# Optimization experiments

Measured on AMD Instinct MI355X. Metric: run time of the kernel, lower is better.

## Reference

```python
import jax, jax.numpy as jnp
import numpy as np

B, S, D, H, M = 4, 2048, 1024, 16, 128
DH = D // H
SCALE = jnp.float32(np.sqrt(D / H))


def setup_inputs() -> dict:
    key = jax.random.key(0)
    ks = jax.random.split(key, 4)
    x = jax.random.normal(ks[0], (B, S, D), dtype=jnp.float32)
    mask = jnp.zeros((B, 1, 1, S), dtype=bool)
    W_in = jax.random.normal(ks[1], (3 * D, D), dtype=jnp.float32) * 0.02
    b_in = jnp.zeros((3 * D,), dtype=jnp.float32)
    pos_emb = jax.random.normal(ks[2], (2 * M + 1, DH), dtype=jnp.float32)
    W_out = jax.random.normal(ks[3], (D, D), dtype=jnp.float32) * 0.02
    b_out = jnp.zeros((D,), dtype=jnp.float32)
    return {"x": x, "mask": mask, "W_in": W_in, "b_in": b_in,
            "pos_emb": pos_emb, "W_out": W_out, "b_out": b_out}


def _arrange_pos(pos_emb, seq_len, max_len):
    k = jnp.arange(seq_len)
    q = jnp.arange(seq_len)
    idx = jnp.clip(k[None, :] - q[:, None], -max_len, max_len) + max_len  # [S,S]
    return pos_emb[idx]  # [S,S,DH]


def reference(x, mask, W_in, b_in, pos_emb, W_out, b_out):
    b, s, d = x.shape
    qkv = x @ W_in.T + b_in                      # [B,S,3D]
    qkv = qkv.reshape(b, s, H, 3 * DH).transpose(0, 2, 1, 3)  # [B,H,S,3DH]
    Q, K, V = jnp.split(qkv, 3, axis=3)          # each [B,H,S,DH]
    logits = jnp.einsum('bhqd,bhkd->bhqk', Q, K)
    rel = _arrange_pos(pos_emb, s, M)            # [S,S,DH] (q,k,dh)
    pos_logits = jnp.einsum('bhqd,qkd->bhqk', Q, rel)
    logits = (logits + pos_logits) / SCALE
    logits = jnp.where(mask, -jnp.inf, logits)
    attn = jax.nn.softmax(logits, axis=3)
    combined = jnp.einsum('bhqk,bhkd->bhqd', attn, V)
    out = combined.transpose(0, 2, 1, 3).reshape(b, s, d)  # concat heads
    return out @ W_out.T + b_out
```

## Files before the change

kernel.cpp:

```cpp
#include <hip/hip_runtime.h>
#include <hip/hip_bf16.h>
#include <math.h>

#define SS 2048
#define HH 16
#define NPOS 257
#define C_SCALE 0.18033688f
#define P_THR 256.0f

typedef short  s16x8 __attribute__((ext_vector_type(8)));
typedef float  f32x4 __attribute__((ext_vector_type(4)));
typedef unsigned u32x4 __attribute__((ext_vector_type(4)));

__device__ __forceinline__ unsigned short f2bf(float f) {
    unsigned u = __builtin_bit_cast(unsigned, f);
    u += 0x7fff + ((u >> 16) & 1);
    return (unsigned short)(u >> 16);
}
__device__ __forceinline__ float bf2f(unsigned short b) {
    return __builtin_bit_cast(float, (unsigned)b << 16);
}
__device__ __forceinline__ s16x8 pack8(float4 a, float4 b) {
    s16x8 v;
    v[0]=(short)f2bf(a.x); v[1]=(short)f2bf(a.y); v[2]=(short)f2bf(a.z); v[3]=(short)f2bf(a.w);
    v[4]=(short)f2bf(b.x); v[5]=(short)f2bf(b.y); v[6]=(short)f2bf(b.z); v[7]=(short)f2bf(b.w);
    return v;
}
__device__ __forceinline__ unsigned cvtpk(float lo, float hi) {
    unsigned r;
    asm("v_cvt_pk_bf16_f32 %0, %1, %2" : "=v"(r) : "v"(lo), "v"(hi));
    return r;
}
__device__ __forceinline__ float exp2_fast(float x) {
    float r;
    asm("v_exp_f32 %0, %1" : "=v"(r) : "v"(x));
    return r;
}
__device__ __forceinline__ f32x4 mfma16(s16x8 a, s16x8 b, f32x4 c) {
    return __builtin_amdgcn_mfma_f32_16x16x32_bf16(a, b, c, 0, 0, 0);
}
__device__ __forceinline__ void gload_lds16(const void* gsrc, void* ldst) {
    __builtin_amdgcn_global_load_lds(
        (const __attribute__((address_space(1))) unsigned int*)gsrc,
        (__attribute__((address_space(3))) unsigned int*)ldst,
        16, 0, 0);
}
__device__ __forceinline__ int colp(int k) {
    return ((k >> 5) << 6) | (((k >> 2) & 3) << 4) | (((k >> 4) & 1) << 3) | ((k & 3) << 1);
}

__global__ __launch_bounds__(256)
void cvt_bf16(const float* __restrict__ in, unsigned short* __restrict__ out, int n8)
{
    for (int i = blockIdx.x * blockDim.x + threadIdx.x; i < n8; i += gridDim.x * blockDim.x) {
        const float4* p = (const float4*)(in + (size_t)i * 8);
        *(s16x8*)(out + (size_t)i * 8) = pack8(p[0], p[1]);
    }
}

__global__ __launch_bounds__(256)
void gemm_bf16_nt(const unsigned short* __restrict__ A,
                  const unsigned short* __restrict__ Bm,
                  const float* __restrict__ bias, float* __restrict__ Cout,
                  int Ndim, int Kdim)
{
    __shared__ short As[128 * 32];
    __shared__ short Bs[128 * 32];
    const int tid  = threadIdx.x;
    const int lane = tid & 63;
    const int wv   = tid >> 6;
    const int g    = lane >> 4;
    const int ln   = lane & 15;
    const int wm   = wv >> 1, wn = wv & 1;
    const int tm   = blockIdx.y << 7, tn = blockIdx.x << 7;
    const int srow  = lane >> 2;
    const int sslot = lane & 3;

    f32x4 acc[4][4];
#pragma unroll
    for (int mi = 0; mi < 4; ++mi)
#pragma unroll
        for (int ni = 0; ni < 4; ++ni) acc[mi][ni] = f32x4{0.f, 0.f, 0.f, 0.f};

    const unsigned short* Ab = A  + (size_t)(tm + wv*32 + srow) * Kdim + sslot*8;
    const unsigned short* Bb = Bm + (size_t)(tn + wv*32 + srow) * Kdim + sslot*8;
    const size_t rstep16 = (size_t)16 * Kdim;
    char* lA = (char*)As + (wv*32) * 64;
    char* lB = (char*)Bs + (wv*32) * 64;

    for (int k0 = 0; k0 < Kdim; k0 += 32) {
        __syncthreads();
        gload_lds16(Ab + k0,           lA);
        gload_lds16(Ab + k0 + rstep16, lA + 1024);
        gload_lds16(Bb + k0,           lB);
        gload_lds16(Bb + k0 + rstep16, lB + 1024);
        __syncthreads();

        s16x8 af[4], bf_[4];
#pragma unroll
        for (int mi = 0; mi < 4; ++mi)
            af[mi] = *(const s16x8*)((char*)As + (wm*64 + mi*16 + ln)*64 + g*16);
#pragma unroll
        for (int ni = 0; ni < 4; ++ni)
            bf_[ni] = *(const s16x8*)((char*)Bs + (wn*64 + ni*16 + ln)*64 + g*16);
#pragma unroll
        for (int mi = 0; mi < 4; ++mi)
#pragma unroll
            for (int ni = 0; ni < 4; ++ni)
                acc[mi][ni] = mfma16(af[mi], bf_[ni], acc[mi][ni]);
    }

#pragma unroll
    for (int ni = 0; ni < 4; ++ni) {
        const int col = tn + wn*64 + ni*16 + ln;
        const float bcol = bias[col];
#pragma unroll
        for (int mi = 0; mi < 4; ++mi)
#pragma unroll
            for (int j = 0; j < 4; ++j) {
                const int row = tm + wm*64 + mi*16 + 4*g + j;
                Cout[(size_t)row * Ndim + col] = acc[mi][ni][j] + bcol;
            }
    }
}

__global__ __launch_bounds__(256)
void gemm_qkv(const unsigned short* __restrict__ A,
              const unsigned short* __restrict__ Bm,
              const float* __restrict__ bias,
              unsigned short* __restrict__ qb,
              char* __restrict__ kbuf, char* __restrict__ vbuf)
{
    __shared__ short As[128 * 32];
    __shared__ short Bs[128 * 32];
    const int tid  = threadIdx.x;
    const int lane = tid & 63;
    const int wv   = tid >> 6;
    const int g    = lane >> 4;
    const int ln   = lane & 15;
    const int wm   = wv >> 1, wn = wv & 1;
    const int tm   = blockIdx.y << 7, tn = blockIdx.x << 7;
    const int srow  = lane >> 2;
    const int sslot = lane & 3;
    const int Kdim = 1024;

    f32x4 acc[4][4];
#pragma unroll
    for (int mi = 0; mi < 4; ++mi)
#pragma unroll
        for (int ni = 0; ni < 4; ++ni) acc[mi][ni] = f32x4{0.f, 0.f, 0.f, 0.f};

    const unsigned short* Ab = A  + (size_t)(tm + wv*32 + srow) * Kdim + sslot*8;
    const unsigned short* Bb = Bm + (size_t)(tn + wv*32 + srow) * Kdim + sslot*8;
    const size_t rstep16 = (size_t)16 * Kdim;
    char* lA = (char*)As + (wv*32) * 64;
    char* lB = (char*)Bs + (wv*32) * 64;

    for (int k0 = 0; k0 < Kdim; k0 += 32) {
        __syncthreads();
        gload_lds16(Ab + k0,           lA);
        gload_lds16(Ab + k0 + rstep16, lA + 1024);
        gload_lds16(Bb + k0,           lB);
        gload_lds16(Bb + k0 + rstep16, lB + 1024);
        __syncthreads();

        s16x8 af[4], bf_[4];
#pragma unroll
        for (int mi = 0; mi < 4; ++mi)
            af[mi] = *(const s16x8*)((char*)As + (wm*64 + mi*16 + ln)*64 + g*16);
#pragma unroll
        for (int ni = 0; ni < 4; ++ni)
            bf_[ni] = *(const s16x8*)((char*)Bs + (wn*64 + ni*16 + ln)*64 + g*16);
#pragma unroll
        for (int mi = 0; mi < 4; ++mi)
#pragma unroll
            for (int ni = 0; ni < 4; ++ni)
                acc[mi][ni] = mfma16(af[mi], bf_[ni], acc[mi][ni]);
    }

#pragma unroll
    for (int ni = 0; ni < 4; ++ni) {
        const int col  = tn + wn*64 + ni*16 + ln;
        const int col0 = tn + wn*64 + ni*16;
        const int h    = col0 / 192;
        const int r0   = col0 - h*192;
        const int r    = r0 + ln;
        const float bcol = bias[col];
#pragma unroll
        for (int mi = 0; mi < 4; ++mi) {
            const int rowb = tm + wm*64 + mi*16 + 4*g;
            const int bb = rowb >> 11, sl = rowb & 2047;
            const int kt = sl >> 6, kr = sl & 63;
            const size_t tile = ((size_t)(bb*HH + h)*32 + kt) * 8192;
            if (r0 < 64) {
                unsigned short* qp = qb + (((size_t)(bb*HH + h))*SS + sl)*64 + r;
#pragma unroll
                for (int j = 0; j < 4; ++j)
                    qp[(size_t)j*64] = f2bf((acc[mi][ni][j] + bcol) * C_SCALE);
            } else if (r0 < 128) {
                const int d = r - 64;
#pragma unroll
                for (int j = 0; j < 4; ++j) {
                    const int krj = kr + j;
                    *(unsigned short*)(kbuf + tile + krj*128 + ((2*d) ^ ((krj&7)<<4))) =
                        f2bf(acc[mi][ni][j] + bcol);
                }
            } else {
                const int d = r - 128;
                uint2 w;
                w.x = cvtpk(acc[mi][ni][0] + bcol, acc[mi][ni][1] + bcol);
                w.y = cvtpk(acc[mi][ni][2] + bcol, acc[mi][ni][3] + bcol);
                *(uint2*)(vbuf + tile + d*128 + (colp(kr) ^ ((d&7)<<4))) = w;
            }
        }
    }
}

#define FAR_LDS  32768
#define NEAR_LDS (16384 + 64*260*2)

__global__ __launch_bounds__(256, 4)
void attn_far(const unsigned short* __restrict__ qb,
              const char* __restrict__ kbuf, const char* __restrict__ vbuf,
              const unsigned short* __restrict__ pos_bf,
              float* __restrict__ o_state,
              float* __restrict__ m_state,
              float* __restrict__ l_state)
{
    extern __shared__ char smem[];
    char* ksb = smem;
    char* vtb = smem + 16384;

    const int tid = threadIdx.x, lane = tid & 63, wv = tid >> 6;
    const int g = lane >> 4, ln = lane & 15;
    const int fid = ((blockIdx.x & 7) << 7) | (blockIdx.x >> 3);
    const int q0 = (fid & 15) << 7, h = (fid >> 4) & 15, b = fid >> 8;
    const int q0w = q0 + wv*32;
    const int swz = (ln & 7) << 4;

    const unsigned short* qhb = qb + ((size_t)(b*HH + h))*SS*64;
    const char* ktile = kbuf + (size_t)(b*HH + h)*32*8192;
    const char* vtile = vbuf + (size_t)(b*HH + h)*32*8192;

    s16x8 qf[2][2];
#pragma unroll
    for (int gg = 0; gg < 2; ++gg) {
        const unsigned short* qp = qhb + (size_t)(q0w + 16*gg + ln) * 64;
        qf[gg][0] = *(const s16x8*)(qp + 8*g);
        qf[gg][1] = *(const s16x8*)(qp + 32 + 8*g);
    }

    const int ktA = max(0, (q0 - 128) >> 6);
    const int ktB = min(32, (q0 + 256) >> 6);
    const int gap = ktB - ktA, nfar = 32 - gap;

    const int kt0 = (ktA > 0) ? 0 : ktB;
    const char* ksrc = ktile + (size_t)(kt0 + 1 == ktA ? ktB : kt0 + 1)*8192 + wv*2048 + lane*16;
    const char* vsrc = vtile + (size_t)(kt0 + 1 == ktA ? ktB : kt0 + 1)*8192 + wv*2048 + lane*16;
    char* kd0 = ksb + wv*2048;         char* kd1 = kd0 + 8192;
    char* vd0 = vtb + wv*2048;         char* vd1 = vd0 + 8192;
    const char* kb0 = ksb + ln*128 + ((g*16) ^ swz);
    const char* kb1 = ksb + ln*128 + ((64 + g*16) ^ swz);
    const char* vb0 = vtb + ln*128 + ((g*16) ^ swz);
    const char* vb1 = vtb + ln*128 + ((64 + g*16) ^ swz);

    {
        const char* s0k = ktile + (size_t)kt0*8192 + wv*2048 + lane*16;
        const char* s0v = vtile + (size_t)kt0*8192 + wv*2048 + lane*16;
        gload_lds16(s0k, kd0); gload_lds16(s0k + 1024, kd0 + 1024);
        gload_lds16(s0v, vd0); gload_lds16(s0v + 1024, vd0 + 1024);
    }

    float blo[2], bhi[2];
    {
        const int bsrc = (ln >> 2) << 4;
        const int s3 = ln & 3;
#pragma unroll
        for (int pass = 0; pass < 2; ++pass) {
            const int c  = pass*256 + ln;
            const int cc = c > 256 ? 256 : c;
            const unsigned short* pp = pos_bf + (size_t)cc * 64;
            s16x8 b0 = *(const s16x8*)(pp + 8*g);
            s16x8 b1 = *(const s16x8*)(pp + 32 + 8*g);
#pragma unroll
            for (int gg = 0; gg < 2; ++gg) {
                f32x4 d = {0,0,0,0};
                d = mfma16(qf[gg][0], b0, d);
                d = mfma16(qf[gg][1], b1, d);
                const float r0 = __shfl(d[0], bsrc, 64);
                const float r1 = __shfl(d[1], bsrc, 64);
                const float r2 = __shfl(d[2], bsrc, 64);
                const float r3 = __shfl(d[3], bsrc, 64);
                const float r = s3 == 0 ? r0 : s3 == 1 ? r1 : s3 == 2 ? r2 : r3;
                if (pass == 0) blo[gg] = r; else bhi[gg] = r;
            }
        }
    }
    __syncthreads();

    f32x4 o[2][4], l[2];
    float m[2];
#pragma unroll
    for (int gg = 0; gg < 2; ++gg) {
        m[gg] = -INFINITY; l[gg] = f32x4{0,0,0,0};
#pragma unroll
        for (int dt = 0; dt < 4; ++dt) o[gg][dt] = f32x4{0,0,0,0};
    }
    s16x8 ONES;
#pragma unroll
    for (int i = 0; i < 8; ++i) ONES[i] = (short)0x3F80;

#define F_TILE(CUR, vv) do {                                                  \
    if ((vv) + 1 < nfar) {                                                    \
        char* dk_ = (CUR) ? kd0 : kd1;                                        \
        char* dv_ = (CUR) ? vd0 : vd1;                                        \
        gload_lds16(ksrc, dk_); gload_lds16(ksrc + 1024, dk_ + 1024);         \
        gload_lds16(vsrc, dv_); gload_lds16(vsrc + 1024, dv_ + 1024);         \
        const int stp_ = (((vv) + 2) == ktA) ? (gap + 1) * 8192 : 8192;       \
        ksrc += stp_; vsrc += stp_;                                           \
    }                                                                         \
    f32x4 s[2][4];                                                            \
    _Pragma("unroll")                                                         \
    for (int gi = 0; gi < 2; ++gi)                                            \
        _Pragma("unroll")                                                     \
        for (int t = 0; t < 4; ++t) s[gi][t] = f32x4{0,0,0,0};                \
    __builtin_amdgcn_s_setprio(1);                                            \
    _Pragma("unroll")                                                         \
    for (int kc = 0; kc < 2; ++kc) {                                          \
        const char* kbx_ = kc ? kb1 : kb0;                                    \
        s16x8 kf[4];                                                          \
        _Pragma("unroll")                                                     \
        for (int t = 0; t < 4; ++t)                                           \
            kf[t] = *(const s16x8*)(kbx_ + (CUR)*8192 + t*2048);              \
        _Pragma("unroll")                                                     \
        for (int t = 0; t < 4; ++t)                                           \
            _Pragma("unroll")                                                 \
            for (int gi = 0; gi < 2; ++gi)                                    \
                s[gi][t] = mfma16(kf[t], qf[gi][kc], s[gi][t]);               \
    }                                                                         \
    __builtin_amdgcn_s_setprio(0);                                            \
    const bool left_ = (vv) < ktA;                                            \
    u32x4 pa[2][2];                                                           \
    float pmax[2];                                                            \
    _Pragma("unroll")                                                         \
    for (int gi = 0; gi < 2; ++gi) {                                          \
        const float bmv = (left_ ? blo[gi] : bhi[gi]) - m[gi];                \
        float pm = 0.f;                                                       \
        _Pragma("unroll")                                                     \
        for (int t = 0; t < 4; ++t) {                                         \
            const float p0 = exp2_fast(s[gi][t][0] + bmv);                    \
            const float p1 = exp2_fast(s[gi][t][1] + bmv);                    \
            const float p2 = exp2_fast(s[gi][t][2] + bmv);                    \
            const float p3 = exp2_fast(s[gi][t][3] + bmv);                    \
            pm = fmaxf(pm, fmaxf(fmaxf(p0, p1), fmaxf(p2, p3)));              \
            pa[gi][t>>1][2*(t&1)]   = cvtpk(p0, p1);                          \
            pa[gi][t>>1][2*(t&1)+1] = cvtpk(p2, p3);                          \
        }                                                                     \
        pmax[gi] = pm;                                                        \
    }                                                                         \
    if (__any(fmaxf(pmax[0], pmax[1]) > P_THR)) {                             \
        _Pragma("unroll")                                                     \
        for (int gi = 0; gi < 2; ++gi) {                                      \
            const float bc = left_ ? blo[gi] : bhi[gi];                       \
            float mr = s[gi][0][0];                                           \
            _Pragma("unroll")                                                 \
            for (int t = 0; t < 4; ++t)                                       \
                _Pragma("unroll")                                             \
                for (int j = 0; j < 4; ++j) mr = fmaxf(mr, s[gi][t][j]);      \
            mr = fmaxf(mr, __shfl_xor(mr, 16, 64));                           \
            mr = fmaxf(mr, __shfl_xor(mr, 32, 64));                           \
            const float nm = fmaxf(m[gi], mr + bc);                           \
            const float corr = exp2_fast(m[gi] - nm);                         \
            m[gi] = nm;                                                       \
            _Pragma("unroll")                                                 \
            for (int j = 0; j < 4; ++j) {                                     \
                const float cj = __shfl(corr, (lane & 48) + 4*g + j, 64);     \
                _Pragma("unroll")                                             \
                for (int dt = 0; dt < 4; ++dt) o[gi][dt][j] *= cj;            \
                l[gi][j] *= cj;                                               \
            }                                                                 \
            const float nb = bc - nm;                                         \
            _Pragma("unroll")                                                 \
            for (int t = 0; t < 4; ++t) {                                     \
                const float p0 = exp2_fast(s[gi][t][0] + nb);                 \
                const float p1 = exp2_fast(s[gi][t][1] + nb);                 \
                const float p2 = exp2_fast(s[gi][t][2] + nb);                 \
                const float p3 = exp2_fast(s[gi][t][3] + nb);                 \
                pa[gi][t>>1][2*(t&1)]   = cvtpk(p0, p1);                      \
                pa[gi][t>>1][2*(t&1)+1] = cvtpk(p2, p3);                      \
            }                                                                 \
        }                                                                     \
    }                                                                         \
    __builtin_amdgcn_s_setprio(1);                                            \
    _Pragma("unroll")                                                         \
    for (int kc = 0; kc < 2; ++kc) {                                          \
        const char* vbx_ = kc ? vb1 : vb0;                                    \
        _Pragma("unroll")                                                     \
        for (int dt = 0; dt < 4; ++dt) {                                      \
            const s16x8 bv = *(const s16x8*)(vbx_ + (CUR)*8192 + dt*2048);    \
            _Pragma("unroll")                                                 \
            for (int gi = 0; gi < 2; ++gi)                                    \
                o[gi][dt] = mfma16(__builtin_bit_cast(s16x8, pa[gi][kc]), bv, o[gi][dt]); \
        }                                                                     \
        _Pragma("unroll")                                                     \
        for (int gi = 0; gi < 2; ++gi)                                        \
            l[gi] = mfma16(__builtin_bit_cast(s16x8, pa[gi][kc]), ONES, l[gi]); \
    }                                                                         \
    __builtin_amdgcn_s_setprio(0);                                            \
    __syncthreads();                                                          \
} while (0)

    for (int v = 0; v < nfar; v += 2) {
        F_TILE(0, v);
        F_TILE(1, v + 1);
    }

    const size_t rbase = (((size_t)(b*HH + h)) << 11) + q0w;
#pragma unroll
    for (int gg = 0; gg < 2; ++gg) {
        if (lane < 16) m_state[rbase + 16*gg + ln] = m[gg];
        if (ln == 0) {
#pragma unroll
            for (int j = 0; j < 4; ++j) l_state[rbase + 16*gg + 4*g + j] = l[gg][j];
        }
#pragma unroll
        for (int dt = 0; dt < 4; ++dt)
#pragma unroll
            for (int j = 0; j < 4; ++j)
                o_state[(rbase + 16*gg + 4*g + j)*64 + dt*16 + ln] = o[gg][dt][j];
    }
}

__global__ __launch_bounds__(256, 3)
void attn_near(const unsigned short* __restrict__ qb,
               const char* __restrict__ kbuf, const char* __restrict__ vbuf,
               const unsigned short* __restrict__ pos_bf,
               const float* __restrict__ o_state,
               const float* __restrict__ m_state,
               const float* __restrict__ l_state,
               unsigned short* __restrict__ comb)
{
    extern __shared__ char smem[];
    char* ksb = smem;
    unsigned short* tab = (unsigned short*)(smem + 16384);

    const int tid = threadIdx.x, lane = tid & 63, wv = tid >> 6;
    const int g = lane >> 4, ln = lane & 15;
    const int fid = ((blockIdx.x & 7) << 8) | (blockIdx.x >> 3);
    const int q0 = (fid & 31) << 6, h = (fid >> 5) & 15, b = fid >> 9;
    const int q0w = q0 + wv*16;
    const int swz = (ln & 7) << 4;

    const unsigned short* qhb = qb + ((size_t)(b*HH + h))*SS*64;
    const char* ktile = kbuf + (size_t)(b*HH + h)*32*8192;
    const char* vtile = vbuf + (size_t)(b*HH + h)*32*8192;

    s16x8 qf[2];
    {
        const unsigned short* qp = qhb + (size_t)(q0w + ln) * 64;
        qf[0] = *(const s16x8*)(qp + 8*g);
        qf[1] = *(const s16x8*)(qp + 32 + 8*g);
    }

    const int q0p = q0 & ~127;
    const int ktA = max(0, (q0p - 128) >> 6);
    const int ktB = min(32, (q0p + 256) >> 6);
    const int ntile = ktB - ktA;

    const char* ksrcN = ktile + (size_t)(ktA + 1)*8192 + wv*2048 + lane*16;
    char* nkd0 = ksb + wv*2048;        char* nkd1 = nkd0 + 8192;
    const char* kb0 = ksb + ln*128 + ((g*16) ^ swz);
    const char* kb1 = ksb + ln*128 + ((64 + g*16) ^ swz);
    const char* vsr0 = vtile + (size_t)ktA*8192 + ln*128 + ((g*16) ^ swz) + 4096;
    const char* vsr1 = vtile + (size_t)ktA*8192 + ln*128 + ((64 + g*16) ^ swz) + 4096;

    s16x8 vf[8];

    {
        const char* s0 = ktile + (size_t)ktA*8192 + wv*2048 + lane*16;
        gload_lds16(s0, nkd0); gload_lds16(s0 + 1024, nkd0 + 1024);
#pragma unroll
        for (int dt = 0; dt < 4; ++dt) {
            vf[dt]     = *(const s16x8*)(vsr0 + dt*2048 - 4096);
            vf[4 + dt] = *(const s16x8*)(vsr1 + dt*2048 - 4096);
        }
        vsr0 += 8192; vsr1 += 8192;
    }

    for (int ct = 0; ct < 17; ++ct) {
        const int c  = ct*16 + ln;
        const int cc = c > 256 ? 256 : c;
        const unsigned short* pp = pos_bf + (size_t)cc * 64;
        s16x8 b0 = *(const s16x8*)(pp + 8*g);
        s16x8 b1 = *(const s16x8*)(pp + 32 + 8*g);
        f32x4 d = {0,0,0,0};
        d = mfma16(qf[0], b0, d);
        d = mfma16(qf[1], b1, d);
        if (c < NPOS) {
#pragma unroll
            for (int j = 0; j < 4; ++j)
                tab[(16*wv + 4*g + j)*260 + c] = f2bf(d[j]);
        }
    }
    __syncthreads();

    const size_t rbase = (((size_t)(b*HH + h)) << 11) + q0w;
    float m_run = m_state[rbase + ln];
    f32x4 l_acc;
#pragma unroll
    for (int j = 0; j < 4; ++j) l_acc[j] = l_state[rbase + 4*g + j];
    f32x4 o_acc[4];
#pragma unroll
    for (int dt = 0; dt < 4; ++dt)
#pragma unroll
        for (int j = 0; j < 4; ++j)
            o_acc[dt][j] = o_state[(rbase + 4*g + j)*64 + dt*16 + ln];

    const int rowb = (16*wv + ln) * 260;
    const int coff = 4*g - 16*wv - ln + 128 - q0;
    s16x8 ONES;
#pragma unroll
    for (int i = 0; i < 8; ++i) ONES[i] = (short)0x3F80;

#define N_TILE(CUR, vv) do {                                                  \
    if ((vv) + 1 < ntile) {                                                   \
        char* d_ = (CUR) ? nkd0 : nkd1;                                       \
        gload_lds16(ksrcN, d_); gload_lds16(ksrcN + 1024, d_ + 1024);         \
        ksrcN += 8192;                                                        \
    }                                                                         \
    f32x4 s[4];                                                               \
    _Pragma("unroll")                                                         \
    for (int t = 0; t < 4; ++t) s[t] = f32x4{0,0,0,0};                        \
    __builtin_amdgcn_s_setprio(1);                                            \
    _Pragma("unroll")                                                         \
    for (int kc = 0; kc < 2; ++kc) {                                          \
        const char* kbx_ = kc ? kb1 : kb0;                                    \
        s16x8 kf[4];                                                          \
        _Pragma("unroll")                                                     \
        for (int t = 0; t < 4; ++t)                                           \
            kf[t] = *(const s16x8*)(kbx_ + (CUR)*8192 + t*2048);              \
        _Pragma("unroll")                                                     \
        for (int t = 0; t < 4; ++t)                                           \
            s[t] = mfma16(kf[t], qf[kc], s[t]);                               \
    }                                                                         \
    __builtin_amdgcn_s_setprio(0);                                            \
    const int colb = ((ktA + (vv)) << 6) + coff;                              \
    _Pragma("unroll")                                                         \
    for (int t = 0; t < 4; ++t)                                               \
        _Pragma("unroll")                                                     \
        for (int j = 0; j < 4; ++j) {                                         \
            int c = colb + 16*t + j;                                          \
            c = c < 0 ? 0 : (c > 256 ? 256 : c);                              \
            s[t][j] = s[t][j] + bf2f(tab[rowb + c]);                          \
        }                                                                     \
    u32x4 pa[2];                                                              \
    float pm = 0.f;                                                           \
    _Pragma("unroll")                                                         \
    for (int t = 0; t < 4; ++t) {                                             \
        const float p0 = exp2_fast(s[t][0] - m_run);                          \
        const float p1 = exp2_fast(s[t][1] - m_run);                          \
        const float p2 = exp2_fast(s[t][2] - m_run);                          \
        const float p3 = exp2_fast(s[t][3] - m_run);                          \
        pm = fmaxf(pm, fmaxf(fmaxf(p0, p1), fmaxf(p2, p3)));                  \
        pa[t>>1][2*(t&1)]   = cvtpk(p0, p1);                                  \
        pa[t>>1][2*(t&1)+1] = cvtpk(p2, p3);                                  \
    }                                                                         \
    if (__any(pm > P_THR)) {                                                  \
        float mr = s[0][0];                                                   \
        _Pragma("unroll")                                                     \
        for (int t = 0; t < 4; ++t)                                           \
            _Pragma("unroll")                                                 \
            for (int j = 0; j < 4; ++j) mr = fmaxf(mr, s[t][j]);              \
        mr = fmaxf(mr, __shfl_xor(mr, 16, 64));                               \
        mr = fmaxf(mr, __shfl_xor(mr, 32, 64));                               \
        const float nm = fmaxf(m_run, mr);                                    \
        const float corr = exp2_fast(m_run - nm);                             \
        m_run = nm;                                                           \
        _Pragma("unroll")                                                     \
        for (int j = 0; j < 4; ++j) {                                         \
            const float cj = __shfl(corr, (lane & 48) + 4*g + j, 64);         \
            _Pragma("unroll")                                                 \
            for (int dt = 0; dt < 4; ++dt) o_acc[dt][j] *= cj;                \
            l_acc[j] *= cj;                                                   \
        }                                                                     \
        _Pragma("unroll")                                                     \
        for (int t = 0; t < 4; ++t) {                                         \
            const float p0 = exp2_fast(s[t][0] - m_run);                      \
            const float p1 = exp2_fast(s[t][1] - m_run);                      \
            const float p2 = exp2_fast(s[t][2] - m_run);                      \
            const float p3 = exp2_fast(s[t][3] - m_run);                      \
            pa[t>>1][2*(t&1)]   = cvtpk(p0, p1);                              \
            pa[t>>1][2*(t&1)+1] = cvtpk(p2, p3);                              \
        }                                                                     \
    }                                                                         \
    __builtin_amdgcn_s_setprio(1);                                            \
    _Pragma("unroll")                                                         \
    for (int kc = 0; kc < 2; ++kc) {                                          \
        const s16x8 pA_ = __builtin_bit_cast(s16x8, pa[kc]);                  \
        _Pragma("unroll")                                                     \
        for (int dt = 0; dt < 4; ++dt)                                        \
            o_acc[dt] = mfma16(pA_, vf[kc*4 + dt], o_acc[dt]);                \
        l_acc = mfma16(pA_, ONES, l_acc);                                     \
    }                                                                         \
    __builtin_amdgcn_s_setprio(0);                                            \
    if ((vv) + 1 < ntile) {                                                   \
        _Pragma("unroll")                                                     \
        for (int dt = 0; dt < 4; ++dt) {                                      \
            vf[dt]     = *(const s16x8*)(vsr0 + dt*2048 - 4096);              \
            vf[4 + dt] = *(const s16x8*)(vsr1 + dt*2048 - 4096);              \
        }                                                                     \
        vsr0 += 8192; vsr1 += 8192;                                           \
    }                                                                         \
    __syncthreads();                                                          \
} while (0)

    for (int v = 0; v < ntile; v += 2) {
        N_TILE(0, v);
        N_TILE(1, v + 1);
    }

    f32x4 inv;
#pragma unroll
    for (int j = 0; j < 4; ++j) inv[j] = 1.0f / l_acc[j];
#pragma unroll
    for (int dt = 0; dt < 4; ++dt)
#pragma unroll
        for (int j = 0; j < 4; ++j)
            comb[((size_t)b*SS + q0w + 4*g + j)*1024 + h*64 + dt*16 + ln] =
                f2bf(o_acc[dt][j] * inv[j]);
}

extern "C" void kernel_launch(void* const* d_in, const int* in_sizes, int n_in,
                              void* d_out, int out_size, void* d_ws, size_t ws_size,
                              hipStream_t stream)
{
    const float* x     = (const float*)d_in[0];
    const float* W_in  = (const float*)d_in[2];
    const float* b_in  = (const float*)d_in[3];
    const float* pos   = (const float*)d_in[4];
    const float* W_out = (const float*)d_in[5];
    const float* b_out = (const float*)d_in[6];
    float* out = (float*)d_out;

    char* ws = (char*)d_ws;
    unsigned short* q_buf   = (unsigned short*)(ws);
    char*           k_buf   = (char*)          (ws +  16777216);
    char*           v_buf   = (char*)          (ws +  33554432);
    unsigned short* comb_bf = (unsigned short*)(ws +  50331648);
    unsigned short* x_bf    = (unsigned short*)(ws +  67108864);
    unsigned short* wi_bf   = (unsigned short*)(ws +  83886080);
    unsigned short* wo_bf   = (unsigned short*)(ws +  90177536);
    unsigned short* pos_bf  = (unsigned short*)(ws +  92274688);
    float*          o_state = (float*)        (ws +  92340224);
    float*          m_state = (float*)        (ws + 125894656);
    float*          l_state = (float*)        (ws + 126418944);

    cvt_bf16<<<2048, 256, 0, stream>>>(x,     x_bf,  8192*1024/8);
    cvt_bf16<<<1024, 256, 0, stream>>>(W_in,  wi_bf, 3072*1024/8);
    cvt_bf16<<<512,  256, 0, stream>>>(W_out, wo_bf, 1024*1024/8);
    cvt_bf16<<<9,    256, 0, stream>>>(pos,   pos_bf, 2056);

    gemm_qkv<<<dim3(24, 64), 256, 0, stream>>>(x_bf, wi_bf, b_in, q_buf, k_buf, v_buf);

    (void)hipFuncSetAttribute((const void*)attn_far,
                              hipFuncAttributeMaxDynamicSharedMemorySize, FAR_LDS);
    attn_far<<<dim3(1024), 256, FAR_LDS, stream>>>(q_buf, k_buf, v_buf, pos_bf,
                                                   o_state, m_state, l_state);

    (void)hipFuncSetAttribute((const void*)attn_near,
                              hipFuncAttributeMaxDynamicSharedMemorySize, NEAR_LDS);
    attn_near<<<dim3(2048), 256, NEAR_LDS, stream>>>(q_buf, k_buf, v_buf, pos_bf,
                                                     o_state, m_state, l_state, comb_bf);

    gemm_bf16_nt<<<dim3(8, 64), 256, 0, stream>>>(comb_bf, wo_bf, b_out, out, 1024, 1024);
}
```

Baseline: 250.6 us.

## Software-pipeline far attention so PV of previous tile overlaps QK softmax

Restructures the far-range attention loop so the P·V MFMAs for tile v-1 are issued right after the QK^T MFMAs for tile v, before the exp/softmax of tile v. This lets matrix-core work overlap the transcendental and VALU softmax work, which previously ran serially. V now uses a triple-buffered LDS ring, so FAR_LDS grows from 32 KB to 40 KB, and a drain step after the loop finishes the last tile. The probabilities of the previous tile must stay live in registers, which raises register pressure and may affect occupancy at the 4-block launch bound.

```diff
diff --git a/kernel.cpp b/kernel.cpp
--- a/kernel.cpp
+++ b/kernel.cpp
@@ -216,7 +216,7 @@
     }
 }
 
-#define FAR_LDS  32768
+#define FAR_LDS  40960
 #define NEAR_LDS (16384 + 64*260*2)
 
 __global__ __launch_bounds__(256, 4)
@@ -255,20 +255,21 @@
     const int gap = ktB - ktA, nfar = 32 - gap;
 
     const int kt0 = (ktA > 0) ? 0 : ktB;
-    const char* ksrc = ktile + (size_t)(kt0 + 1 == ktA ? ktB : kt0 + 1)*8192 + wv*2048 + lane*16;
-    const char* vsrc = vtile + (size_t)(kt0 + 1 == ktA ? ktB : kt0 + 1)*8192 + wv*2048 + lane*16;
-    char* kd0 = ksb + wv*2048;         char* kd1 = kd0 + 8192;
-    char* vd0 = vtb + wv*2048;         char* vd1 = vd0 + 8192;
-    const char* kb0 = ksb + ln*128 + ((g*16) ^ swz);
-    const char* kb1 = ksb + ln*128 + ((64 + g*16) ^ swz);
-    const char* vb0 = vtb + ln*128 + ((g*16) ^ swz);
-    const char* vb1 = vtb + ln*128 + ((64 + g*16) ^ swz);
+    const int kt1 = (kt0 + 1 == ktA) ? ktB : kt0 + 1;
+    const char* ksrc = ktile + (size_t)kt1*8192 + wv*2048 + lane*16;
+    const char* vsrc = vtile + (size_t)kt1*8192 + wv*2048 + lane*16;
+    const char* kbse0 = ksb + ln*128 + ((g*16) ^ swz);
+    const char* kbse1 = ksb + ln*128 + ((64 + g*16) ^ swz);
+    const char* vbse0 = vtb + ln*128 + ((g*16) ^ swz);
+    const char* vbse1 = vtb + ln*128 + ((64 + g*16) ^ swz);
 
     {
         const char* s0k = ktile + (size_t)kt0*8192 + wv*2048 + lane*16;
         const char* s0v = vtile + (size_t)kt0*8192 + wv*2048 + lane*16;
-        gload_lds16(s0k, kd0); gload_lds16(s0k + 1024, kd0 + 1024);
-        gload_lds16(s0v, vd0); gload_lds16(s0v + 1024, vd0 + 1024);
+        char* dk = ksb + wv*2048;
+        char* dv = vtb + wv*2048;
+        gload_lds16(s0k, dk); gload_lds16(s0k + 1024, dk + 1024);
+        gload_lds16(s0v, dv); gload_lds16(s0v + 1024, dv + 1024);
     }
 
     float blo[2], bhi[2];
@@ -310,110 +311,128 @@
 #pragma unroll
     for (int i = 0; i < 8; ++i) ONES[i] = (short)0x3F80;
 
-#define F_TILE(CUR, vv) do {                                                  \
-    if ((vv) + 1 < nfar) {                                                    \
-        char* dk_ = (CUR) ? kd0 : kd1;                                        \
-        char* dv_ = (CUR) ? vd0 : vd1;                                        \
-        gload_lds16(ksrc, dk_); gload_lds16(ksrc + 1024, dk_ + 1024);         \
-        gload_lds16(vsrc, dv_); gload_lds16(vsrc + 1024, dv_ + 1024);         \
-        const int stp_ = (((vv) + 2) == ktA) ? (gap + 1) * 8192 : 8192;       \
-        ksrc += stp_; vsrc += stp_;                                           \
-    }                                                                         \
-    f32x4 s[2][4];                                                            \
-    _Pragma("unroll")                                                         \
-    for (int gi = 0; gi < 2; ++gi)                                            \
-        _Pragma("unroll")                                                     \
-        for (int t = 0; t < 4; ++t) s[gi][t] = f32x4{0,0,0,0};                \
-    __builtin_amdgcn_s_setprio(1);                                            \
-    _Pragma("unroll")                                                         \
-    for (int kc = 0; kc < 2; ++kc) {                                          \
-        const char* kbx_ = kc ? kb1 : kb0;                                    \
-        s16x8 kf[4];                                                          \
-        _Pragma("unroll")                                                     \
-        for (int t = 0; t < 4; ++t)                                           \
-            kf[t] = *(const s16x8*)(kbx_ + (CUR)*8192 + t*2048);              \
-        _Pragma("unroll")                                                     \
-        for (int t = 0; t < 4; ++t)                                           \
-            _Pragma("unroll")                                                 \
-            for (int gi = 0; gi < 2; ++gi)                                    \
-                s[gi][t] = mfma16(kf[t], qf[gi][kc], s[gi][t]);               \
-    }                                                                         \
-    __builtin_amdgcn_s_setprio(0);                                            \
-    const bool left_ = (vv) < ktA;                                            \
-    u32x4 pa[2][2];                                                           \
-    float pmax[2];                                                            \
-    _Pragma("unroll")                                                         \
-    for (int gi = 0; gi < 2; ++gi) {                                          \
-        const float bmv = (left_ ? blo[gi] : bhi[gi]) - m[gi];                \
-        float pm = 0.f;                                                       \
-        _Pragma("unroll")                                                     \
-        for (int t = 0; t < 4; ++t) {                                         \
-            const float p0 = exp2_fast(s[gi][t][0] + bmv);                    \
-            const float p1 = exp2_fast(s[gi][t][1] + bmv);                    \
-            const float p2 = exp2_fast(s[gi][t][2] + bmv);                    \
-            const float p3 = exp2_fast(s[gi][t][3] + bmv);                    \
-            pm = fmaxf(pm, fmaxf(fmaxf(p0, p1), fmaxf(p2, p3)));              \
-            pa[gi][t>>1][2*(t&1)]   = cvtpk(p0, p1);                          \
-            pa[gi][t>>1][2*(t&1)+1] = cvtpk(p2, p3);                          \
-        }                                                                     \
-        pmax[gi] = pm;                                                        \
-    }                                                                         \
-    if (__any(fmaxf(pmax[0], pmax[1]) > P_THR)) {                             \
-        _Pragma("unroll")                                                     \
-        for (int gi = 0; gi < 2; ++gi) {                                      \
-            const float bc = left_ ? blo[gi] : bhi[gi];                       \
-            float mr = s[gi][0][0];                                           \
-            _Pragma("unroll")                                                 \
-            for (int t = 0; t < 4; ++t)                                       \
-                _Pragma("unroll")                                             \
-                for (int j = 0; j < 4; ++j) mr = fmaxf(mr, s[gi][t][j]);      \
-            mr = fmaxf(mr, __shfl_xor(mr, 16, 64));                           \
-            mr = fmaxf(mr, __shfl_xor(mr, 32, 64));                           \
-            const float nm = fmaxf(m[gi], mr + bc);                           \
-            const float corr = exp2_fast(m[gi] - nm);                         \
-            m[gi] = nm;                                                       \
-            _Pragma("unroll")                                                 \
-            for (int j = 0; j < 4; ++j) {                                     \
-                const float cj = __shfl(corr, (lane & 48) + 4*g + j, 64);     \
-                _Pragma("unroll")                                             \
-                for (int dt = 0; dt < 4; ++dt) o[gi][dt][j] *= cj;            \
-                l[gi][j] *= cj;                                               \
-            }                                                                 \
-            const float nb = bc - nm;                                         \
-            _Pragma("unroll")                                                 \
-            for (int t = 0; t < 4; ++t) {                                     \
-                const float p0 = exp2_fast(s[gi][t][0] + nb);                 \
-                const float p1 = exp2_fast(s[gi][t][1] + nb);                 \
-                const float p2 = exp2_fast(s[gi][t][2] + nb);                 \
-                const float p3 = exp2_fast(s[gi][t][3] + nb);                 \
-                pa[gi][t>>1][2*(t&1)]   = cvtpk(p0, p1);                      \
-                pa[gi][t>>1][2*(t&1)+1] = cvtpk(p2, p3);                      \
-            }                                                                 \
-        }                                                                     \
-    }                                                                         \
-    __builtin_amdgcn_s_setprio(1);                                            \
-    _Pragma("unroll")                                                         \
-    for (int kc = 0; kc < 2; ++kc) {                                          \
-        const char* vbx_ = kc ? vb1 : vb0;                                    \
-        _Pragma("unroll")                                                     \
-        for (int dt = 0; dt < 4; ++dt) {                                      \
-            const s16x8 bv = *(const s16x8*)(vbx_ + (CUR)*8192 + dt*2048);    \
-            _Pragma("unroll")                                                 \
-            for (int gi = 0; gi < 2; ++gi)                                    \
-                o[gi][dt] = mfma16(__builtin_bit_cast(s16x8, pa[gi][kc]), bv, o[gi][dt]); \
-        }                                                                     \
-        _Pragma("unroll")                                                     \
-        for (int gi = 0; gi < 2; ++gi)                                        \
-            l[gi] = mfma16(__builtin_bit_cast(s16x8, pa[gi][kc]), ONES, l[gi]); \
-    }                                                                         \
-    __builtin_amdgcn_s_setprio(0);                                            \
-    __syncthreads();                                                          \
-} while (0)
-
-    for (int v = 0; v < nfar; v += 2) {
-        F_TILE(0, v);
-        F_TILE(1, v + 1);
-    }
+    u32x4 paP[2][2];
+    int ivp = 2, ivc = 0, ivn = 1;
+
+    for (int v = 0; v < nfar; ++v) {
+        if (v + 1 < nfar) {
+            char* dk = ksb + ((v + 1) & 1)*8192 + wv*2048;
+            char* dv = vtb + ivn*8192 + wv*2048;
+            gload_lds16(ksrc, dk); gload_lds16(ksrc + 1024, dk + 1024);
+            gload_lds16(vsrc, dv); gload_lds16(vsrc + 1024, dv + 1024);
+            const int stp = ((v + 2) == ktA) ? (gap + 1) * 8192 : 8192;
+            ksrc += stp; vsrc += stp;
+        }
+
+        f32x4 s[2][4];
+#pragma unroll
+        for (int gi = 0; gi < 2; ++gi)
+#pragma unroll
+            for (int t = 0; t < 4; ++t) s[gi][t] = f32x4{0,0,0,0};
+        __builtin_amdgcn_s_setprio(1);
+#pragma unroll
+        for (int kc = 0; kc < 2; ++kc) {
+            const char* kbx = (kc ? kbse1 : kbse0) + (v & 1)*8192;
+            s16x8 kf[4];
+#pragma unroll
+            for (int t = 0; t < 4; ++t)
+                kf[t] = *(const s16x8*)(kbx + t*2048);
+#pragma unroll
+            for (int t = 0; t < 4; ++t)
+#pragma unroll
+                for (int gi = 0; gi < 2; ++gi)
+                    s[gi][t] = mfma16(kf[t], qf[gi][kc], s[gi][t]);
+        }
+        if (v > 0) {
+#pragma unroll
+            for (int kc = 0; kc < 2; ++kc) {
+                const char* vbx = (kc ? vbse1 : vbse0) + ivp*8192;
+#pragma unroll
+                for (int dt = 0; dt < 4; ++dt) {
+                    const s16x8 bv = *(const s16x8*)(vbx + dt*2048);
+#pragma unroll
+                    for (int gi = 0; gi < 2; ++gi)
+                        o[gi][dt] = mfma16(__builtin_bit_cast(s16x8, paP[gi][kc]), bv, o[gi][dt]);
+                }
+#pragma unroll
+                for (int gi = 0; gi < 2; ++gi)
+                    l[gi] = mfma16(__builtin_bit_cast(s16x8, paP[gi][kc]), ONES, l[gi]);
+            }
+        }
+        __builtin_amdgcn_s_setprio(0);
+
+        const bool left_ = v < ktA;
+        float pmax[2];
+#pragma unroll
+        for (int gi = 0; gi < 2; ++gi) {
+            const float bmv = (left_ ? blo[gi] : bhi[gi]) - m[gi];
+            float pm = 0.f;
+#pragma unroll
+            for (int t = 0; t < 4; ++t) {
+                const float p0 = exp2_fast(s[gi][t][0] + bmv);
+                const float p1 = exp2_fast(s[gi][t][1] + bmv);
+                const float p2 = exp2_fast(s[gi][t][2] + bmv);
+                const float p3 = exp2_fast(s[gi][t][3] + bmv);
+                pm = fmaxf(pm, fmaxf(fmaxf(p0, p1), fmaxf(p2, p3)));
+                paP[gi][t>>1][2*(t&1)]   = cvtpk(p0, p1);
+                paP[gi][t>>1][2*(t&1)+1] = cvtpk(p2, p3);
+            }
+            pmax[gi] = pm;
+        }
+        if (__any(fmaxf(pmax[0], pmax[1]) > P_THR)) {
+#pragma unroll
+            for (int gi = 0; gi < 2; ++gi) {
+                const float bc = left_ ? blo[gi] : bhi[gi];
+                float mr = s[gi][0][0];
+#pragma unroll
+                for (int t = 0; t < 4; ++t)
+#pragma unroll
+                    for (int j = 0; j < 4; ++j) mr = fmaxf(mr, s[gi][t][j]);
+                mr = fmaxf(mr, __shfl_xor(mr, 16, 64));
+                mr = fmaxf(mr, __shfl_xor(mr, 32, 64));
+                const float nm = fmaxf(m[gi], mr + bc);
+                const float corr = exp2_fast(m[gi] - nm);
+                m[gi] = nm;
+#pragma unroll
+                for (int j = 0; j < 4; ++j) {
+                    const float cj = __shfl(corr, (lane & 48) + 4*g + j, 64);
+#pragma unroll
+                    for (int dt = 0; dt < 4; ++dt) o[gi][dt][j] *= cj;
+                    l[gi][j] *= cj;
+                }
+                const float nb = bc - nm;
+#pragma unroll
+                for (int t = 0; t < 4; ++t) {
+                    const float p0 = exp2_fast(s[gi][t][0] + nb);
+                    const float p1 = exp2_fast(s[gi][t][1] + nb);
+                    const float p2 = exp2_fast(s[gi][t][2] + nb);
+                    const float p3 = exp2_fast(s[gi][t][3] + nb);
+                    paP[gi][t>>1][2*(t&1)]   = cvtpk(p0, p1);
+                    paP[gi][t>>1][2*(t&1)+1] = cvtpk(p2, p3);
+                }
+            }
+        }
+
+        ivp = ivc; ivc = ivn; ivn = (ivn + 1 == 3) ? 0 : ivn + 1;
+        __syncthreads();
+    }
+
+    __builtin_amdgcn_s_setprio(1);
+#pragma unroll
+    for (int kc = 0; kc < 2; ++kc) {
+        const char* vbx = (kc ? vbse1 : vbse0) + ivp*8192;
+#pragma unroll
+        for (int dt = 0; dt < 4; ++dt) {
+            const s16x8 bv = *(const s16x8*)(vbx + dt*2048);
+#pragma unroll
+            for (int gi = 0; gi < 2; ++gi)
+                o[gi][dt] = mfma16(__builtin_bit_cast(s16x8, paP[gi][kc]), bv, o[gi][dt]);
+        }
+#pragma unroll
+        for (int gi = 0; gi < 2; ++gi)
+            l[gi] = mfma16(__builtin_bit_cast(s16x8, paP[gi][kc]), ONES, l[gi]);
+    }
+    __builtin_amdgcn_s_setprio(0);
 
     const size_t rbase = (((size_t)(b*HH + h)) << 11) + q0w;
 #pragma unroll
```

After: 255.3 us. Within noise of the previous version (+1.9%).

## Prefetch two K/V tiles ahead with explicit vmcnt waits and raw barriers

Applied to the files above, without the earlier changes.

Restructures the far-tile attention loop so two K/V tiles are loaded into LDS before the loop starts. The next tile's global-to-LDS load is now issued after the current tile's compute and barrier, and partial s_waitcnt vmcnt counts replace the full __syncthreads drain. The aim is to keep more memory traffic in flight so tile loads overlap with MFMA and softmax work. The cost is an extra barrier per tile and hand-written waitcnt/sched_barrier code whose correctness depends on the counts matching the issued loads.

```diff
diff --git a/kernel.cpp b/kernel.cpp
--- a/kernel.cpp
+++ b/kernel.cpp
@@ -254,22 +254,29 @@
     const int ktB = min(32, (q0 + 256) >> 6);
     const int gap = ktB - ktA, nfar = 32 - gap;
 
-    const int kt0 = (ktA > 0) ? 0 : ktB;
-    const char* ksrc = ktile + (size_t)(kt0 + 1 == ktA ? ktB : kt0 + 1)*8192 + wv*2048 + lane*16;
-    const char* vsrc = vtile + (size_t)(kt0 + 1 == ktA ? ktB : kt0 + 1)*8192 + wv*2048 + lane*16;
     char* kd0 = ksb + wv*2048;         char* kd1 = kd0 + 8192;
     char* vd0 = vtb + wv*2048;         char* vd1 = vd0 + 8192;
-    const char* kb0 = ksb + ln*128 + ((g*16) ^ swz);
-    const char* kb1 = ksb + ln*128 + ((64 + g*16) ^ swz);
-    const char* vb0 = vtb + ln*128 + ((g*16) ^ swz);
-    const char* vb1 = vtb + ln*128 + ((64 + g*16) ^ swz);
+    const char* kbse0 = ksb + ln*128 + ((g*16) ^ swz);
+    const char* kbse1 = ksb + ln*128 + ((64 + g*16) ^ swz);
+    const char* vbse0 = vtb + ln*128 + ((g*16) ^ swz);
+    const char* vbse1 = vtb + ln*128 + ((64 + g*16) ^ swz);
+
+    const int sq0 = (ktA > 0) ? 0 : gap;
+    const int sq1 = (1 < ktA) ? 1 : 1 + gap;
+    const int sq2 = (2 < ktA) ? 2 : 2 + gap;
 
     {
-        const char* s0k = ktile + (size_t)kt0*8192 + wv*2048 + lane*16;
-        const char* s0v = vtile + (size_t)kt0*8192 + wv*2048 + lane*16;
+        const char* s0k = ktile + (size_t)sq0*8192 + wv*2048 + lane*16;
+        const char* s0v = vtile + (size_t)sq0*8192 + wv*2048 + lane*16;
         gload_lds16(s0k, kd0); gload_lds16(s0k + 1024, kd0 + 1024);
         gload_lds16(s0v, vd0); gload_lds16(s0v + 1024, vd0 + 1024);
-    }
+        const char* s1k = ktile + (size_t)sq1*8192 + wv*2048 + lane*16;
+        const char* s1v = vtile + (size_t)sq1*8192 + wv*2048 + lane*16;
+        gload_lds16(s1k, kd1); gload_lds16(s1k + 1024, kd1 + 1024);
+        gload_lds16(s1v, vd1); gload_lds16(s1v + 1024, vd1 + 1024);
+    }
+    const char* ksrc = ktile + (size_t)sq2*8192 + wv*2048 + lane*16;
+    const char* vsrc = vtile + (size_t)sq2*8192 + wv*2048 + lane*16;
 
     float blo[2], bhi[2];
     {
@@ -296,7 +303,6 @@
             }
         }
     }
-    __syncthreads();
 
     f32x4 o[2][4], l[2];
     float m[2];
@@ -310,15 +316,13 @@
 #pragma unroll
     for (int i = 0; i < 8; ++i) ONES[i] = (short)0x3F80;
 
+    asm volatile("s_waitcnt vmcnt(4)" ::: "memory");
+    __builtin_amdgcn_sched_barrier(0);
+    __builtin_amdgcn_s_barrier();
+    __builtin_amdgcn_sched_barrier(0);
+
 #define F_TILE(CUR, vv) do {                                                  \
-    if ((vv) + 1 < nfar) {                                                    \
-        char* dk_ = (CUR) ? kd0 : kd1;                                        \
-        char* dv_ = (CUR) ? vd0 : vd1;                                        \
-        gload_lds16(ksrc, dk_); gload_lds16(ksrc + 1024, dk_ + 1024);         \
-        gload_lds16(vsrc, dv_); gload_lds16(vsrc + 1024, dv_ + 1024);         \
-        const int stp_ = (((vv) + 2) == ktA) ? (gap + 1) * 8192 : 8192;       \
-        ksrc += stp_; vsrc += stp_;                                           \
-    }                                                                         \
+                                  \
     f32x4 s[2][4];                                                            \
     _Pragma("unroll")                                                         \
     for (int gi = 0; gi < 2; ++gi)                                            \
@@ -327,11 +331,11 @@
     __builtin_amdgcn_s_setprio(1);                                            \
     _Pragma("unroll")                                                         \
     for (int kc = 0; kc < 2; ++kc) {                                          \
-        const char* kbx_ = kc ? kb1 : kb0;                                    \
+        const char* kbx_ = (kc ? kbse1 : kbse0) + (CUR)*8192;                 \
         s16x8 kf[4];                                                          \
         _Pragma("unroll")                                                     \
         for (int t = 0; t < 4; ++t)                                           \
-            kf[t] = *(const s16x8*)(kbx_ + (CUR)*8192 + t*2048);              \
+            kf[t] = *(const s16x8*)(kbx_ + t*2048);                           \
         _Pragma("unroll")                                                     \
         for (int t = 0; t < 4; ++t)                                           \
             _Pragma("unroll")                                                 \
@@ -358,7 +362,7 @@
         }                                                                     \
         pmax[gi] = pm;                                                        \
     }                                                                         \
-    if (__any(fmaxf(pmax[0], pmax[1]) > P_THR)) {                             \
+    if (__any(fmaxf(pmax[0], pmax[1]) > P_THR)) {           \
         _Pragma("unroll")                                                     \
         for (int gi = 0; gi < 2; ++gi) {                                      \
             const float bc = left_ ? blo[gi] : bhi[gi];                       \
@@ -394,10 +398,10 @@
     __builtin_amdgcn_s_setprio(1);                                            \
     _Pragma("unroll")                                                         \
     for (int kc = 0; kc < 2; ++kc) {                                          \
-        const char* vbx_ = kc ? vb1 : vb0;                                    \
+        const char* vbx_ = (kc ? vbse1 : vbse0) + (CUR)*8192;                 \
         _Pragma("unroll")                                                     \
         for (int dt = 0; dt < 4; ++dt) {                                      \
-            const s16x8 bv = *(const s16x8*)(vbx_ + (CUR)*8192 + dt*2048);    \
+            const s16x8 bv = *(const s16x8*)(vbx_ + dt*2048);                 \
             _Pragma("unroll")                                                 \
             for (int gi = 0; gi < 2; ++gi)                                    \
                 o[gi][dt] = mfma16(__builtin_bit_cast(s16x8, pa[gi][kc]), bv, o[gi][dt]); \
@@ -407,7 +411,26 @@
             l[gi] = mfma16(__builtin_bit_cast(s16x8, pa[gi][kc]), ONES, l[gi]); \
     }                                                                         \
     __builtin_amdgcn_s_setprio(0);                                            \
-    __syncthreads();                                                          \
+                                     \
+    __builtin_amdgcn_s_barrier();                                             \
+    __builtin_amdgcn_sched_barrier(0);                                        \
+                                \
+    if ((vv) + 2 < nfar) {                                                    \
+        char* dk_ = (CUR) ? kd1 : kd0;                                        \
+        char* dv_ = (CUR) ? vd1 : vd0;                                        \
+        gload_lds16(ksrc, dk_); gload_lds16(ksrc + 1024, dk_ + 1024);         \
+        gload_lds16(vsrc, dv_); gload_lds16(vsrc + 1024, dv_ + 1024);         \
+        const int stp_ = (((vv) + 3) == ktA) ? (gap + 1) * 8192 : 8192;       \
+        ksrc += stp_; vsrc += stp_;                                           \
+    }                                                                         \
+     \
+    if ((vv) + 1 < nfar) {                                                    \
+        if ((vv) + 2 < nfar) { asm volatile("s_waitcnt vmcnt(4)" ::: "memory"); } \
+        else                 { asm volatile("s_waitcnt vmcnt(0)" ::: "memory"); } \
+        __builtin_amdgcn_sched_barrier(0);                                    \
+        __builtin_amdgcn_s_barrier();                                         \
+        __builtin_amdgcn_sched_barrier(0);                                    \
+    }                                                                         \
 } while (0)
 
     for (int v = 0; v < nfar; v += 2) {
```

Measured after the change: 250.5 us. No clear change (-0.0%).
